# Kernel optimization log

Measured on AMD Instinct MI355X. Metric: run time of the kernel, lower is better.

Reference implementation:

```python
import jax, jax.numpy as jnp
import numpy as np

S, B, C, H, DH = 16, 16, 256, 4, 64
HW_TABLE, HW_HAND = 256, 36
HW = HW_TABLE + HW_HAND + 1  # 293 spatial tokens (table + hand + global)
LK = 128
MAX_T = 64
UH, UW, UC = 4, 4, 2
TH, TW, HH, HWW = 16, 16, 6, 6
N_MODES, N_SHAPES, N_COLORS = 20, 64, 16


def _ln(x, g, b):
    m = jnp.mean(x, -1, keepdims=True)
    v = jnp.var(x, -1, keepdims=True)
    return (x - m) / jnp.sqrt(v + 1e-5) * g + b


def _forward(tq, pad_q, xk, tk, pad_k,
             spatial_enc, temporal_enc, ln1_g, ln1_b,
             wq, bq, wk, bk, wv, bv, wo, bo, ln2_g, ln2_b,
             w1, b1, w2, b2, table_w, table_b, hand_w, hand_b,
             mode_w, mode_b, shape_w, shape_b, color_w, color_b):
    s, b = tq.shape
    Lq = s * HW
    # temporal + spatial positional broadcast-add -> padded query stream
    xt = temporal_enc[tq]                                        # (s,b,C)
    xq = (xt[:, None] + spatial_enc[None, :, None]).reshape(Lq, b, C)
    tq_e = jnp.broadcast_to(tq[:, None], (s, HW, b)).reshape(Lq, b)
    # padded causal mask: key visible iff tk <= tq, key in pad_k, query in pad_q*HW
    allowed = ((tk[None] <= tq_e[:, None])
               & (jnp.arange(LK)[None, :, None] < pad_k[None, None])
               & (jnp.arange(Lq)[:, None, None] < (pad_q * HW)[None, None]))  # (Lq,Lk,b)
    # cross-attention TransformerBlock (pre-LN MHA + FFN)
    qn = _ln(xq, ln1_g, ln1_b)
    Q = (qn @ wq + bq).reshape(Lq, b, H, DH)
    K = (xk @ wk + bk).reshape(LK, b, H, DH)
    V = (xk @ wv + bv).reshape(LK, b, H, DH)
    scores = jnp.einsum('qbhd,kbhd->bhqk', Q, K) / np.float32(np.sqrt(DH))
    scores = jnp.where(jnp.transpose(allowed, (2, 0, 1))[:, None], scores, jnp.float32(-1e9))
    a = jnp.einsum('bhqk,kbhd->qbhd', jax.nn.softmax(scores, -1), V).reshape(Lq, b, C)
    x = xq + a @ wo + bo
    x = x + jax.nn.gelu(_ln(x, ln2_g, ln2_b) @ w1 + b1) @ w2 + b2
    x = x.reshape(s, HW, b, C)
    # table decode: pixel-unshuffle (s,th,tw,b,uh,uw,uc) -> (s,b,uc,th*uh,tw*uw)
    tx = x[:, :HW_TABLE] @ table_w + table_b
    tx = tx.reshape(s, TH, TW, b, UH, UW, UC).transpose(0, 3, 6, 1, 4, 2, 5)
    tx = tx.reshape(s, b, UC, TH * UH, TW * UW)
    hx = x[:, HW_TABLE:HW_TABLE + HW_HAND] @ hand_w + hand_b
    hx = hx.reshape(s, HH, HWW, b, UH, UW, UC).transpose(0, 3, 6, 1, 4, 2, 5)
    hx = hx.reshape(s, b, UC, HH * UH, HWW * UW)
    gx = x[:, HW - 1]  # (s,b,C) global token
    return (gx @ mode_w + mode_b, gx @ shape_w + shape_b, gx @ color_w + color_b, tx, hx)


def setup_inputs():
    ks = jax.random.split(jax.random.key(0), 40)
    p = lambda k, shp: jax.random.normal(k, shp, jnp.float32) * 0.02
    inp = {}
    inp['tq'] = jnp.sort(jax.random.randint(ks[0], (S, B), 0, MAX_T), axis=0)
    inp['pad_q'] = jax.random.randint(ks[1], (B,), S // 2, S + 1)
    inp['xk'] = jax.random.normal(ks[2], (LK, B, C), jnp.float32)
    inp['tk'] = jnp.sort(jax.random.randint(ks[3], (LK, B), 0, MAX_T), axis=0).at[0].set(0)
    inp['pad_k'] = jax.random.randint(ks[4], (B,), LK // 2, LK + 1)
    inp['table_cursor_activate'] = jax.random.randint(ks[5], (S, B), 0, 2)
    inp['hand_cursor_activate'] = jax.random.randint(ks[6], (S, B), 0, 2)
    inp['insert_activate'] = jax.random.randint(ks[7], (S, B), 0, 2)
    inp['spatial_enc'] = p(ks[8], (HW, C))
    inp['temporal_enc'] = p(ks[9], (MAX_T, C))
    inp['ln1_g'] = jnp.ones(C); inp['ln1_b'] = jnp.zeros(C)
    inp['wq'] = p(ks[10], (C, C)); inp['bq'] = jnp.zeros(C)
    inp['wk'] = p(ks[11], (C, C)); inp['bk'] = jnp.zeros(C)
    inp['wv'] = p(ks[12], (C, C)); inp['bv'] = jnp.zeros(C)
    inp['wo'] = p(ks[13], (C, C)); inp['bo'] = jnp.zeros(C)
    inp['ln2_g'] = jnp.ones(C); inp['ln2_b'] = jnp.zeros(C)
    inp['w1'] = p(ks[14], (C, 4 * C)); inp['b1'] = jnp.zeros(4 * C)
    inp['w2'] = p(ks[15], (4 * C, C)); inp['b2'] = jnp.zeros(C)
    inp['table_w'] = p(ks[16], (C, UH * UW * UC)); inp['table_b'] = jnp.zeros(UH * UW * UC)
    inp['hand_w'] = p(ks[17], (C, UH * UW * UC)); inp['hand_b'] = jnp.zeros(UH * UW * UC)
    inp['mode_w'] = p(ks[18], (C, N_MODES)); inp['mode_b'] = jnp.zeros(N_MODES)
    inp['shape_w'] = p(ks[19], (C, N_SHAPES)); inp['shape_b'] = jnp.zeros(N_SHAPES)
    inp['color_w'] = p(ks[20], (C, N_COLORS)); inp['color_b'] = jnp.zeros(N_COLORS)
    return inp


def reference(tq, pad_q, xk, tk, pad_k, table_cursor_activate, hand_cursor_activate,
              insert_activate, spatial_enc, temporal_enc, ln1_g, ln1_b,
              wq, bq, wk, bk, wv, bv, wo, bo, ln2_g, ln2_b,
              w1, b1, w2, b2, table_w, table_b, hand_w, hand_b,
              mode_w, mode_b, shape_w, shape_b, color_w, color_b):
    # cursor/insert activates are unused in the old_style branch
    return _forward(tq, pad_q, xk, tk, pad_k, spatial_enc, temporal_enc,
                    ln1_g, ln1_b, wq, bq, wk, bk, wv, bv, wo, bo, ln2_g, ln2_b,
                    w1, b1, w2, b2, table_w, table_b, hand_w, hand_b,
                    mode_w, mode_b, shape_w, shape_b, color_w, color_b)
```

## Files before the change

### kernel.cpp

```cpp
#include <hip/hip_runtime.h>
#include <hip/hip_bf16.h>

namespace {
constexpr int cS = 16, cB = 16, cC = 256, cH = 4, cDH = 64, cHW = 293;
constexpr int cLQ = cS * cHW;
constexpr int cLK = 128;
constexpr int cNN = cLQ * cB;
constexpr size_t TX_OFF = 25600;
constexpr size_t HX_OFF = 2122752;
}

typedef unsigned short ushort_t;
typedef unsigned int uint_t;
typedef __attribute__((ext_vector_type(8))) short short8;
typedef __attribute__((ext_vector_type(4))) float f32x4;

__device__ __forceinline__ float bf2f(ushort_t u) {
  return __uint_as_float(((uint_t)u) << 16);
}
__device__ __forceinline__ ushort_t f2bf(float f) {
  __hip_bfloat16 h = __float2bfloat16(f);
  return *(ushort_t*)&h;
}

__device__ __forceinline__ size_t swz(int r, int c) {
  return (((size_t)(r >> 4) * 8 + (c >> 5)) * 64 + ((c >> 3) & 3) * 16 + (r & 15)) * 8 + (c & 7);
}

__global__ __launch_bounds__(256) void k_prep(
    const float* __restrict__ xk, ushort_t* __restrict__ xkb,
    const float* __restrict__ wq, ushort_t* __restrict__ wqs,
    const float* __restrict__ wk, ushort_t* __restrict__ wks,
    const float* __restrict__ wv, ushort_t* __restrict__ wvs,
    const float* __restrict__ wo, ushort_t* __restrict__ wos,
    const float* __restrict__ w1, ushort_t* __restrict__ w1s,
    const float* __restrict__ w2, ushort_t* __restrict__ w2s,
    const float* __restrict__ tw, ushort_t* __restrict__ tws,
    const float* __restrict__ hw_, ushort_t* __restrict__ hws)
{
  int bid = blockIdx.x;
  if (bid < 512) {
    int i4 = bid * 256 + threadIdx.x;
    int r = i4 >> 6;
    int c0 = (i4 & 63) * 4;
    float4 v = *(const float4*)(xk + (size_t)r * 256 + c0);
    ushort_t o[4] = {f2bf(v.x), f2bf(v.y), f2bf(v.z), f2bf(v.w)};
    *(uint2*)&xkb[swz(r, c0)] = *(uint2*)o;
    return;
  }
  int rr = bid - 512;
  const float* W; ushort_t* Ws; int N; int lb;
  if      (rr < 32)  { W = wq;  Ws = wqs; N = 256;  lb = rr; }
  else if (rr < 64)  { W = wk;  Ws = wks; N = 256;  lb = rr - 32; }
  else if (rr < 96)  { W = wv;  Ws = wvs; N = 256;  lb = rr - 64; }
  else if (rr < 128) { W = wo;  Ws = wos; N = 256;  lb = rr - 96; }
  else if (rr < 256) { W = w1;  Ws = w1s; N = 1024; lb = rr - 128; }
  else if (rr < 384) { W = w2;  Ws = w2s; N = 256;  lb = rr - 256; }
  else if (rr < 388) { W = tw;  Ws = tws; N = 32;   lb = rr - 384; }
  else               { W = hw_; Ws = hws; N = 32;   lb = rr - 388; }
  int slot = lb * 256 + threadIdx.x;
  int lane = slot & 63;
  int fr   = slot >> 6;
  int NB   = N >> 4;
  int nb   = fr % NB, kc = fr / NB;
  int n    = nb * 16 + (lane & 15);
  int k0   = kc * 32 + (lane >> 4) * 8;
  ushort_t tmp[8];
  #pragma unroll
  for (int i = 0; i < 8; ++i) tmp[i] = f2bf(W[(size_t)(k0 + i) * N + n]);
  *(uint4*)&Ws[(size_t)slot * 8] = *(uint4*)tmp;
}

__device__ __forceinline__ void gemm_k256(
    const ushort_t* __restrict__ A, const ushort_t* __restrict__ Ws,
    int rt0, int slot0, int NB, int lane, f32x4 c[4][4])
{
  #pragma unroll 2
  for (int kc = 0; kc < 8; ++kc) {
    short8 a[4];
    #pragma unroll
    for (int mf = 0; mf < 4; ++mf)
      a[mf] = *(const short8*)(A + (((size_t)(rt0 + mf) * 8 + kc) * 64 + lane) * 8);
    #pragma unroll
    for (int nb = 0; nb < 4; ++nb) {
      short8 b = *(const short8*)(Ws + (((size_t)kc * NB + slot0 + nb) * 64 + lane) * 8);
      #pragma unroll
      for (int mf = 0; mf < 4; ++mf)
        c[mf][nb] = __builtin_amdgcn_mfma_f32_16x16x32_bf16(a[mf], b, c[mf][nb], 0, 0, 0);
    }
  }
}

__global__ __launch_bounds__(256, 4) void k_qnp(
    const int* __restrict__ tq, const float* __restrict__ spatial,
    const float* __restrict__ temporal, const float* __restrict__ g,
    const float* __restrict__ bt, const ushort_t* __restrict__ Ws,
    const float* __restrict__ Bi, ushort_t* __restrict__ Out)
{
  __shared__ ushort_t aT[64 * 256];
  const int tid = threadIdx.x, lane = tid & 63, w = tid >> 6;
  const int rt0 = blockIdx.x * 4, row0 = blockIdx.x * 64;
  {
    int q = rt0 + w;
    int s = q / cHW, hw = q % cHW;
    int c0 = lane * 4;
    float4 sv = *(const float4*)(spatial + (size_t)hw * cC + c0);
    float4 g4 = *(const float4*)(g + c0);
    float4 b4 = *(const float4*)(bt + c0);
    int kc = c0 >> 5, qq = (c0 >> 3) & 3, joff = c0 & 7;
    for (int rr = 0; rr < 16; ++rr) {
      int t = tq[s * cB + rr];
      float4 tv = *(const float4*)(temporal + (size_t)t * cC + c0);
      float v0 = tv.x + sv.x, v1 = tv.y + sv.y, v2 = tv.z + sv.z, v3 = tv.w + sv.w;
      float sum = v0 + v1 + v2 + v3;
      float sum2 = v0 * v0 + v1 * v1 + v2 * v2 + v3 * v3;
      #pragma unroll
      for (int off = 32; off >= 1; off >>= 1) {
        sum  += __shfl_xor(sum,  off, 64);
        sum2 += __shfl_xor(sum2, off, 64);
      }
      float mean = sum * (1.0f / cC);
      float var  = sum2 * (1.0f / cC) - mean * mean;
      float inv  = rsqrtf(var + 1e-5f);
      ushort_t o[4] = {f2bf((v0 - mean) * inv * g4.x + b4.x),
                       f2bf((v1 - mean) * inv * g4.y + b4.y),
                       f2bf((v2 - mean) * inv * g4.z + b4.z),
                       f2bf((v3 - mean) * inv * g4.w + b4.w)};
      *(uint2*)&aT[(((w * 8 + kc) * 64) + qq * 16 + rr) * 8 + joff] = *(uint2*)o;
    }
  }
  __syncthreads();
  f32x4 z = {0.f, 0.f, 0.f, 0.f};
  f32x4 c[4][4];
  #pragma unroll
  for (int mf = 0; mf < 4; ++mf)
    #pragma unroll
    for (int nb = 0; nb < 4; ++nb) c[mf][nb] = z;
  gemm_k256(aT, Ws, 0, w * 4, 16, lane, c);
  const int lane15 = lane & 15, kq = lane >> 4;
  __syncthreads();
  #pragma unroll
  for (int nb = 0; nb < 4; ++nb) {
    int col = w * 64 + nb * 16 + lane15;
    float bias = Bi[col];
    #pragma unroll
    for (int mf = 0; mf < 4; ++mf)
      #pragma unroll
      for (int i = 0; i < 4; ++i)
        aT[(mf * 16 + kq * 4 + i) * 256 + col] = f2bf(c[mf][nb][i] + bias);
  }
  __syncthreads();
  uint2* outp = (uint2*)(Out + (size_t)row0 * 256);
  #pragma unroll
  for (int it = 0; it < 16; ++it) {
    int f = tid + it * 256;
    int row = f >> 6, c0 = (f & 63) * 4;
    outp[f] = *(uint2*)&aT[row * 256 + c0];
  }
}

__global__ __launch_bounds__(256, 4) void k_kv(
    const ushort_t* __restrict__ xkb, const ushort_t* __restrict__ wks,
    const ushort_t* __restrict__ wvs, const float* __restrict__ bk,
    const float* __restrict__ bv, ushort_t* __restrict__ Kb,
    ushort_t* __restrict__ Vb)
{
  const ushort_t* Ws = blockIdx.y ? wvs : wks;
  const float* Bi = blockIdx.y ? bv : bk;
  ushort_t* Out = blockIdx.y ? Vb : Kb;
  const int lane = threadIdx.x & 63, w = threadIdx.x >> 6;
  const int rt0 = blockIdx.x * 4, row0 = blockIdx.x * 64;
  f32x4 z = {0.f, 0.f, 0.f, 0.f};
  f32x4 c[4][4];
  #pragma unroll
  for (int mf = 0; mf < 4; ++mf)
    #pragma unroll
    for (int nb = 0; nb < 4; ++nb) c[mf][nb] = z;
  gemm_k256(xkb, Ws, rt0, w * 4, 16, lane, c);
  const int lane15 = lane & 15, kq = lane >> 4;
  #pragma unroll
  for (int nb = 0; nb < 4; ++nb) {
    int col = w * 64 + nb * 16 + lane15;
    float bias = Bi[col];
    #pragma unroll
    for (int mf = 0; mf < 4; ++mf)
      #pragma unroll
      for (int i = 0; i < 4; ++i) {
        int row = row0 + mf * 16 + kq * 4 + i;
        Out[(size_t)row * 256 + col] = f2bf(c[mf][nb][i] + bias);
      }
  }
}

__global__ __launch_bounds__(512, 4) void k_woffn(
    const ushort_t* __restrict__ A, const ushort_t* __restrict__ wos,
    const float* __restrict__ bo, const int* __restrict__ tq,
    const float* __restrict__ spatial, const float* __restrict__ temporal,
    const float* __restrict__ g, const float* __restrict__ bt,
    const ushort_t* __restrict__ w1s, const float* __restrict__ b1,
    const ushort_t* __restrict__ w2s, const float* __restrict__ b2,
    ushort_t* xres, ushort_t* __restrict__ x2out)
{
  __shared__ ushort_t aT[64 * 256];
  __shared__ ushort_t hL[64 * 256];
  __shared__ float red[8][64][2];
  __shared__ float meanL[64], invL[64];
  const int tid = threadIdx.x, lane = tid & 63, w = tid >> 6;
  const int lane15 = lane & 15, kq = lane >> 4;
  const int rt0 = blockIdx.x * 4, row0 = blockIdx.x * 64;
  const f32x4 z = {0.f, 0.f, 0.f, 0.f};

  f32x4 c[4][2];
  #pragma unroll
  for (int mf = 0; mf < 4; ++mf)
    #pragma unroll
    for (int nb = 0; nb < 2; ++nb) c[mf][nb] = z;
  #pragma unroll 1
  for (int kc = 0; kc < 8; ++kc) {
    short8 a[4];
    #pragma unroll
    for (int mf = 0; mf < 4; ++mf)
      a[mf] = *(const short8*)(A + (((size_t)(rt0 + mf) * 8 + kc) * 64 + lane) * 8);
    #pragma unroll
    for (int nb = 0; nb < 2; ++nb) {
      short8 b = *(const short8*)(wos + (((size_t)kc * 16 + w * 2 + nb) * 64 + lane) * 8);
      #pragma unroll
      for (int mf = 0; mf < 4; ++mf)
        c[mf][nb] = __builtin_amdgcn_mfma_f32_16x16x32_bf16(a[mf], b, c[mf][nb], 0, 0, 0);
    }
  }
  {
    int tt[4][4], hws[4];
    #pragma unroll
    for (int mf = 0; mf < 4; ++mf) {
      int q = rt0 + mf;
      int s = q / cHW;
      hws[mf] = q % cHW;
      #pragma unroll
      for (int i = 0; i < 4; ++i) tt[mf][i] = tq[s * cB + kq * 4 + i];
    }
    #pragma unroll
    for (int nb = 0; nb < 2; ++nb) {
      int col = w * 32 + nb * 16 + lane15;
      float bias = bo[col];
      #pragma unroll
      for (int mf = 0; mf < 4; ++mf) {
        float sp = spatial[(size_t)hws[mf] * cC + col];
        #pragma unroll
        for (int i = 0; i < 4; ++i)
          c[mf][nb][i] += bias + temporal[(size_t)tt[mf][i] * cC + col] + sp;
      }
    }
  }
  #pragma unroll
  for (int mf = 0; mf < 4; ++mf)
    #pragma unroll
    for (int i = 0; i < 4; ++i) {
      float s4 = c[mf][0][i] + c[mf][1][i];
      float q4 = c[mf][0][i] * c[mf][0][i] + c[mf][1][i] * c[mf][1][i];
      #pragma unroll
      for (int off = 8; off >= 1; off >>= 1) {
        s4 += __shfl_xor(s4, off, 64);
        q4 += __shfl_xor(q4, off, 64);
      }
      if (lane15 == 0) {
        red[w][mf * 16 + kq * 4 + i][0] = s4;
        red[w][mf * 16 + kq * 4 + i][1] = q4;
      }
    }
  __syncthreads();
  if (tid < 64) {
    float S = 0.f, Q = 0.f;
    #pragma unroll
    for (int ww = 0; ww < 8; ++ww) { S += red[ww][tid][0]; Q += red[ww][tid][1]; }
    float m = S * (1.0f / cC);
    float v = Q * (1.0f / cC) - m * m;
    meanL[tid] = m;
    invL[tid] = rsqrtf(v + 1e-5f);
  }
  __syncthreads();
  #pragma unroll
  for (int nb = 0; nb < 2; ++nb) {
    int col = w * 32 + nb * 16 + lane15;
    float gc = g[col], bc = bt[col];
    int qd = nb * 2 + (lane15 >> 3);
    int jd = lane15 & 7;
    #pragma unroll
    for (int mf = 0; mf < 4; ++mf)
      #pragma unroll
      for (int i = 0; i < 4; ++i) {
        int rl = mf * 16 + kq * 4 + i;
        float val = c[mf][nb][i];
        float lv = (val - meanL[rl]) * invL[rl] * gc + bc;
        aT[((mf * 8 + w) * 64 + qd * 16 + kq * 4 + i) * 8 + jd] = f2bf(lv);
        hL[rl * 256 + col] = f2bf(val);
      }
  }
  __syncthreads();
  {
    uint2* xw = (uint2*)(xres + (size_t)row0 * 256);
    #pragma unroll
    for (int it = 0; it < 8; ++it) {
      int f = tid + it * 512;
      int row = f >> 6, c0 = (f & 63) * 4;
      xw[f] = *(uint2*)&hL[row * 256 + c0];
    }
  }
  f32x4 c2[4][2];
  #pragma unroll
  for (int mf = 0; mf < 4; ++mf)
    #pragma unroll
    for (int nb = 0; nb < 2; ++nb) c2[mf][nb] = z;
  for (int hc = 0; hc < 4; ++hc) {
    f32x4 c1[4][2];
    #pragma unroll
    for (int mf = 0; mf < 4; ++mf)
      #pragma unroll
      for (int nb = 0; nb < 2; ++nb) c1[mf][nb] = z;
    #pragma unroll 1
    for (int kc = 0; kc < 8; ++kc) {
      short8 a[4];
      #pragma unroll
      for (int mf = 0; mf < 4; ++mf)
        a[mf] = *(const short8*)&aT[((mf * 8 + kc) * 64 + lane) * 8];
      #pragma unroll
      for (int nb = 0; nb < 2; ++nb) {
        int slot = hc * 16 + w * 2 + nb;
        short8 b = *(const short8*)(w1s + (((size_t)kc * 64 + slot) * 64 + lane) * 8);
        #pragma unroll
        for (int mf = 0; mf < 4; ++mf)
          c1[mf][nb] = __builtin_amdgcn_mfma_f32_16x16x32_bf16(a[mf], b, c1[mf][nb], 0, 0, 0);
      }
    }
    __syncthreads();
    #pragma unroll
    for (int nb = 0; nb < 2; ++nb) {
      int k2l = w * 32 + nb * 16 + lane15;
      float bias = b1[hc * 256 + k2l];
      int kc2l = k2l >> 5, kq2 = (k2l >> 3) & 3, j2 = k2l & 7;
      #pragma unroll
      for (int mf = 0; mf < 4; ++mf)
        #pragma unroll
        for (int i = 0; i < 4; ++i) {
          float xx = c1[mf][nb][i] + bias;
          float x2v = xx * xx;
          float mm = fmaf(x2v, 0.044715f, 1.0f);
          float u2 = xx * mm * -1.5957691216057308f;
          float e = __expf(u2);
          float ge = xx * __builtin_amdgcn_rcpf(1.0f + e);
          hL[(((kc2l * 4 + mf) * 64) + kq2 * 16 + kq * 4 + i) * 8 + j2] = f2bf(ge);
        }
    }
    __syncthreads();
    #pragma unroll 1
    for (int kc2 = 0; kc2 < 8; ++kc2) {
      short8 a2[4];
      #pragma unroll
      for (int mf = 0; mf < 4; ++mf)
        a2[mf] = *(const short8*)&hL[((kc2 * 4 + mf) * 64 + lane) * 8];
      #pragma unroll
      for (int nb = 0; nb < 2; ++nb) {
        short8 b = *(const short8*)(w2s +
            (((size_t)(hc * 8 + kc2) * 16 + w * 2 + nb) * 64 + lane) * 8);
        #pragma unroll
        for (int mf = 0; mf < 4; ++mf)
          c2[mf][nb] = __builtin_amdgcn_mfma_f32_16x16x32_bf16(a2[mf], b, c2[mf][nb], 0, 0, 0);
      }
    }
  }
  __syncthreads();
  #pragma unroll
  for (int nb = 0; nb < 2; ++nb) {
    int col = w * 32 + nb * 16 + lane15;
    float bias = b2[col];
    #pragma unroll
    for (int mf = 0; mf < 4; ++mf)
      #pragma unroll
      for (int i = 0; i < 4; ++i)
        aT[(mf * 16 + kq * 4 + i) * 256 + col] = f2bf(c2[mf][nb][i] + bias);
  }
  __syncthreads();
  {
    const int rt = (tid + 256) & 511;
    uint2* xp = (uint2*)(x2out + (size_t)row0 * 256);
    const uint2* xr = (const uint2*)(xres + (size_t)row0 * 256);
    #pragma unroll
    for (int it = 0; it < 8; ++it) {
      int f = rt + it * 512;
      int row = f >> 6, c0 = (f & 63) * 4;
      uint2 hv = *(uint2*)&aT[row * 256 + c0];
      uint2 rv = xr[f];
      const ushort_t* hp = (const ushort_t*)&hv;
      const ushort_t* rp = (const ushort_t*)&rv;
      ushort_t o[4];
      #pragma unroll
      for (int j = 0; j < 4; ++j) o[j] = f2bf(bf2f(hp[j]) + bf2f(rp[j]));
      xp[f] = *(uint2*)o;
    }
  }
}

__global__ __launch_bounds__(512, 4) void k_attn(
    const ushort_t* __restrict__ Qb, const ushort_t* __restrict__ Kb,
    const ushort_t* __restrict__ Vb, const int* __restrict__ tq,
    const int* __restrict__ tk, const int* __restrict__ pad_q,
    const int* __restrict__ pad_k, ushort_t* __restrict__ aout)
{
  __shared__ ushort_t KL[128 * 72];
  __shared__ ushort_t VtL[64 * 136];
  __shared__ ushort_t pL[8][16 * 136];
  __shared__ int tkL[128];

  const int h = blockIdx.y, b = blockIdx.z;
  const int tid = threadIdx.x, lane = tid & 63, w = tid >> 6;
  const int m15 = lane & 15, quad = lane >> 4;

  for (int i = tid; i < 128 * 16; i += 512) {
    int k = i >> 4, d4 = (i & 15) * 4;
    size_t src = (size_t)(k * cB + b) * 256 + h * 64 + d4;
    uint2 kv = *(const uint2*)&Kb[src];
    uint2 vv = *(const uint2*)&Vb[src];
    *(uint2*)&KL[k * 72 + d4] = kv;
    const ushort_t* vvp = (const ushort_t*)&vv;
    #pragma unroll
    for (int t = 0; t < 4; ++t) VtL[(d4 + t) * 136 + k] = vvp[t];
  }
  if (tid < 128) tkL[tid] = tk[tid * cB + b];
  __syncthreads();
  const int pk = pad_k[b];
  const int pq = pad_q[b] * cHW;
  ushort_t* pRow = pL[w];
  const f32x4 z = {0.f, 0.f, 0.f, 0.f};

  for (int pr = 0; pr < 4; ++pr) {
    int qt = blockIdx.x * 32 + pr * 8 + w;
    if (qt >= 293) break;
    const ushort_t* qrow =
        Qb + ((size_t)((qt * 16 + m15) * cB + b)) * 256 + h * 64 + quad * 8;
    short8 qa0 = *(const short8*)(qrow);
    short8 qa1 = *(const short8*)(qrow + 32);
    f32x4 s[8];
    #pragma unroll
    for (int nf = 0; nf < 8; ++nf) {
      const ushort_t* kp = KL + (nf * 16 + m15) * 72 + quad * 8;
      short8 b0 = *(const short8*)(kp);
      short8 b1 = *(const short8*)(kp + 32);
      s[nf] = __builtin_amdgcn_mfma_f32_16x16x32_bf16(qa0, b0, z, 0, 0, 0);
      s[nf] = __builtin_amdgcn_mfma_f32_16x16x32_bf16(qa1, b1, s[nf], 0, 0, 0);
    }
    int tqv[4], qok[4];
    #pragma unroll
    for (int i = 0; i < 4; ++i) {
      int qg = qt * 16 + quad * 4 + i;
      int sidx = (qg * 3579) >> 20;
      tqv[i] = tq[sidx * cB + b];
      qok[i] = (qg < pq);
    }
    #pragma unroll
    for (int nf = 0; nf < 8; ++nf) {
      int kidx = nf * 16 + m15;
      int tkc = tkL[kidx];
      bool kok = (kidx < pk);
      #pragma unroll
      for (int i = 0; i < 4; ++i) {
        bool ok = kok && qok[i] && (tkc <= tqv[i]);
        s[nf][i] = ok ? s[nf][i] * 0.125f : -1e9f;
      }
    }
    float mx[4], l[4];
    #pragma unroll
    for (int i = 0; i < 4; ++i) {
      float m = s[0][i];
      #pragma unroll
      for (int nf = 1; nf < 8; ++nf) m = fmaxf(m, s[nf][i]);
      #pragma unroll
      for (int off = 8; off >= 1; off >>= 1) m = fmaxf(m, __shfl_xor(m, off, 64));
      mx[i] = m;
    }
    #pragma unroll
    for (int i = 0; i < 4; ++i) l[i] = 0.f;
    #pragma unroll
    for (int nf = 0; nf < 8; ++nf)
      #pragma unroll
      for (int i = 0; i < 4; ++i) {
        float p = __expf(s[nf][i] - mx[i]);
        s[nf][i] = p;
        l[i] += p;
      }
    #pragma unroll
    for (int i = 0; i < 4; ++i) {
      float t = l[i];
      #pragma unroll
      for (int off = 8; off >= 1; off >>= 1) t += __shfl_xor(t, off, 64);
      l[i] = 1.0f / t;
    }
    #pragma unroll
    for (int nf = 0; nf < 8; ++nf)
      #pragma unroll
      for (int i = 0; i < 4; ++i)
        pRow[(quad * 4 + i) * 136 + nf * 16 + m15] = f2bf(s[nf][i]);
    f32x4 o[4];
    #pragma unroll
    for (int nf = 0; nf < 4; ++nf) o[nf] = z;
    #pragma unroll
    for (int kc = 0; kc < 4; ++kc) {
      short8 pa = *(const short8*)(pRow + m15 * 136 + kc * 32 + quad * 8);
      #pragma unroll
      for (int nf = 0; nf < 4; ++nf) {
        short8 vb = *(const short8*)(VtL + (nf * 16 + m15) * 136 + kc * 32 + quad * 8);
        o[nf] = __builtin_amdgcn_mfma_f32_16x16x32_bf16(pa, vb, o[nf], 0, 0, 0);
      }
    }
    #pragma unroll
    for (int nf = 0; nf < 4; ++nf) {
      int c = h * 64 + nf * 16 + m15;
      size_t base = ((size_t)(c >> 5)) * 64 + ((c >> 3) & 3) * 16 + b;
      int cj = c & 7;
      #pragma unroll
      for (int i = 0; i < 4; ++i) {
        int qg = qt * 16 + quad * 4 + i;
        aout[(((size_t)qg * 8) * 64 + base) * 8 + cj] = f2bf(o[nf][i] * l[i]);
      }
    }
  }
}

__global__ __launch_bounds__(256, 4) void k_thm(
    const ushort_t* __restrict__ x2, const ushort_t* __restrict__ tws,
    const float* __restrict__ tb, const ushort_t* __restrict__ hws,
    const float* __restrict__ hb, float* __restrict__ out)
{
  __shared__ ushort_t aT[64 * 264];
  const int tid = threadIdx.x, lane = tid & 63, w = tid >> 6;
  const int m15 = lane & 15, quad = lane >> 4;
  const int row0 = blockIdx.x * 64;
  #pragma unroll
  for (int it = 0; it < 8; ++it) {
    int f = tid + it * 256;
    int row = f >> 5, cb = f & 31;
    *(uint4*)&aT[row * 264 + cb * 8] =
        *(const uint4*)&x2[(size_t)(row0 + row) * 256 + cb * 8];
  }
  __syncthreads();
  const f32x4 z = {0.f, 0.f, 0.f, 0.f};
  f32x4 ct[2], ch[2];
  ct[0] = ct[1] = ch[0] = ch[1] = z;
  const ushort_t* arow = aT + (w * 16 + m15) * 264 + quad * 8;
  #pragma unroll
  for (int kc = 0; kc < 8; ++kc) {
    short8 a = *(const short8*)(arow + kc * 32);
    #pragma unroll
    for (int nb = 0; nb < 2; ++nb) {
      short8 bt_ = *(const short8*)(tws + (((size_t)(kc * 2 + nb)) * 64 + lane) * 8);
      short8 bh_ = *(const short8*)(hws + (((size_t)(kc * 2 + nb)) * 64 + lane) * 8);
      ct[nb] = __builtin_amdgcn_mfma_f32_16x16x32_bf16(a, bt_, ct[nb], 0, 0, 0);
      ch[nb] = __builtin_amdgcn_mfma_f32_16x16x32_bf16(a, bh_, ch[nb], 0, 0, 0);
    }
  }
  #pragma unroll
  for (int nb = 0; nb < 2; ++nb) {
    int j = nb * 16 + m15;
    float tbias = tb[j], hbias = hb[j];
    int uh = j >> 3, uw = (j >> 1) & 3, uc = j & 1;
    #pragma unroll
    for (int i = 0; i < 4; ++i) {
      int rg = row0 + w * 16 + quad * 4 + i;
      int b = rg & 15, q = rg >> 4;
      int s = (q * 3579) >> 20;
      int hw = q - s * cHW;
      if (hw < 256) {
        int th = hw >> 4, twi = hw & 15;
        size_t idx = TX_OFF +
            ((((size_t)(s * cB + b)) * 2 + uc) * 64 + (th * 4 + uh)) * 64 + (twi * 4 + uw);
        out[idx] = ct[nb][i] + tbias;
      } else if (hw < 292) {
        int h2 = hw - 256;
        int hh = h2 / 6, ww = h2 % 6;
        size_t idx = HX_OFF +
            ((((size_t)(s * cB + b)) * 2 + uc) * 24 + (hh * 4 + uh)) * 24 + (ww * 4 + uw);
        out[idx] = ch[nb][i] + hbias;
      }
    }
  }
}

__global__ __launch_bounds__(128) void k_gx(
    const ushort_t* __restrict__ x2,
    const float* __restrict__ mw, const float* __restrict__ mbi,
    const float* __restrict__ sw, const float* __restrict__ sbi,
    const float* __restrict__ cw, const float* __restrict__ cbi,
    float* __restrict__ out)
{
  int sb = blockIdx.x;
  int s = sb >> 4, b = sb & 15;
  __shared__ float rowL[256];
  const ushort_t* row = x2 + ((size_t)(s * cHW + 292) * cB + b) * cC;
  for (int i = threadIdx.x; i < 256; i += 128) rowL[i] = bf2f(row[i]);
  __syncthreads();
  int j = threadIdx.x;
  if (j < 100) {
    const float* W;
    const float* Bi;
    int jj, M;
    size_t off;
    if (j < 20)      { W = mw; Bi = mbi; jj = j;      M = 20; off = 0;     }
    else if (j < 84) { W = sw; Bi = sbi; jj = j - 20; M = 64; off = 5120;  }
    else             { W = cw; Bi = cbi; jj = j - 84; M = 16; off = 21504; }
    float acc = Bi[jj];
    for (int c = 0; c < 256; ++c) acc = fmaf(rowL[c], W[c * M + jj], acc);
    out[off + (size_t)sb * M + jj] = acc;
  }
}

extern "C" void kernel_launch(void* const* d_in, const int* in_sizes, int n_in,
                              void* d_out, int out_size, void* d_ws, size_t ws_size,
                              hipStream_t stream)
{
  const int*   tq       = (const int*)d_in[0];
  const int*   pad_q    = (const int*)d_in[1];
  const float* xk       = (const float*)d_in[2];
  const int*   tk       = (const int*)d_in[3];
  const int*   pad_k    = (const int*)d_in[4];
  const float* spatial  = (const float*)d_in[8];
  const float* temporal = (const float*)d_in[9];
  const float* ln1_g    = (const float*)d_in[10];
  const float* ln1_b    = (const float*)d_in[11];
  const float* wq       = (const float*)d_in[12];
  const float* bq       = (const float*)d_in[13];
  const float* wk       = (const float*)d_in[14];
  const float* bk       = (const float*)d_in[15];
  const float* wv       = (const float*)d_in[16];
  const float* bv       = (const float*)d_in[17];
  const float* wo       = (const float*)d_in[18];
  const float* bo       = (const float*)d_in[19];
  const float* ln2_g    = (const float*)d_in[20];
  const float* ln2_b    = (const float*)d_in[21];
  const float* w1       = (const float*)d_in[22];
  const float* b1       = (const float*)d_in[23];
  const float* w2       = (const float*)d_in[24];
  const float* b2       = (const float*)d_in[25];
  const float* table_w  = (const float*)d_in[26];
  const float* table_b  = (const float*)d_in[27];
  const float* hand_w   = (const float*)d_in[28];
  const float* hand_b   = (const float*)d_in[29];
  const float* mode_w   = (const float*)d_in[30];
  const float* mode_b   = (const float*)d_in[31];
  const float* shape_w  = (const float*)d_in[32];
  const float* shape_b  = (const float*)d_in[33];
  const float* color_w  = (const float*)d_in[34];
  const float* color_b  = (const float*)d_in[35];
  float* out = (float*)d_out;

  char* ws = (char*)d_ws;
  const size_t NB2 = (size_t)cNN * cC * sizeof(ushort_t);
  ushort_t* buf1 = (ushort_t*)ws;
  ushort_t* buf2 = (ushort_t*)(ws + NB2);
  char* p = ws + 2 * NB2;
  ushort_t* Kb  = (ushort_t*)p;  p += (size_t)cLK * cB * 256 * 2;
  ushort_t* Vb  = (ushort_t*)p;  p += (size_t)cLK * cB * 256 * 2;
  ushort_t* xkb = (ushort_t*)p;  p += (size_t)cLK * cB * 256 * 2;
  ushort_t* wqs = (ushort_t*)p;  p += 256 * 256 * 2;
  ushort_t* wks = (ushort_t*)p;  p += 256 * 256 * 2;
  ushort_t* wvs = (ushort_t*)p;  p += 256 * 256 * 2;
  ushort_t* wos = (ushort_t*)p;  p += 256 * 256 * 2;
  ushort_t* w1s = (ushort_t*)p;  p += 256 * 1024 * 2;
  ushort_t* w2s = (ushort_t*)p;  p += 1024 * 256 * 2;
  ushort_t* tws = (ushort_t*)p;  p += 256 * 32 * 2;
  ushort_t* hws = (ushort_t*)p;  p += 256 * 32 * 2;

  k_prep<<<904, 256, 0, stream>>>(xk, xkb, wq, wqs, wk, wks, wv, wvs,
                                  wo, wos, w1, w1s, w2, w2s,
                                  table_w, tws, hand_w, hws);
  k_kv<<<dim3(32, 2), 256, 0, stream>>>(xkb, wks, wvs, bk, bv, Kb, Vb);
  k_qnp<<<cNN / 64, 256, 0, stream>>>(tq, spatial, temporal, ln1_g, ln1_b,
                                      wqs, bq, buf2);
  k_attn<<<dim3(10, cH, cB), 512, 0, stream>>>(buf2, Kb, Vb, tq, tk,
                                               pad_q, pad_k, buf1);
  k_woffn<<<cNN / 64, 512, 0, stream>>>(buf1, wos, bo, tq, spatial, temporal,
                                        ln2_g, ln2_b, w1s, b1, w2s, b2,
                                        buf1, buf2);
  k_thm<<<cNN / 64, 256, 0, stream>>>(buf2, tws, table_b, hws, hand_b, out);
  k_gx<<<cS * cB, 128, 0, stream>>>(buf2, mode_w, mode_b, shape_w, shape_b,
                                    color_w, color_b, out);
}
```

Before: 435.1 us.

## Split FFN first GEMM into halves and merge global heads into table/hand kernel

In the fused Wo+FFN kernel, each 256-wide hidden chunk is now computed in two 16-column halves, with the GELU write for each half issued right after it. This halves the live c1 accumulator registers, which may help occupancy, and lets the first half's GELU overlap the second half's MFMAs. Separately, the small mode/shape/color head kernel is folded into the table/hand decode kernel as extra blocks, removing one launch. The extra blocks use the 256-thread shape, so some threads sit idle in the tail work.

```diff
diff --git a/kernel.cpp b/kernel.cpp
--- a/kernel.cpp
+++ b/kernel.cpp
@@ -312,44 +312,41 @@
     #pragma unroll
     for (int nb = 0; nb < 2; ++nb) c2[mf][nb] = z;
   for (int hc = 0; hc < 4; ++hc) {
-    f32x4 c1[4][2];
-    #pragma unroll
-    for (int mf = 0; mf < 4; ++mf)
-      #pragma unroll
-      for (int nb = 0; nb < 2; ++nb) c1[mf][nb] = z;
-    #pragma unroll 1
-    for (int kc = 0; kc < 8; ++kc) {
-      short8 a[4];
-      #pragma unroll
-      for (int mf = 0; mf < 4; ++mf)
-        a[mf] = *(const short8*)&aT[((mf * 8 + kc) * 64 + lane) * 8];
-      #pragma unroll
-      for (int nb = 0; nb < 2; ++nb) {
-        int slot = hc * 16 + w * 2 + nb;
+    #pragma unroll
+    for (int half = 0; half < 2; ++half) {
+      f32x4 c1[4];
+      #pragma unroll
+      for (int mf = 0; mf < 4; ++mf) c1[mf] = z;
+      #pragma unroll 1
+      for (int kc = 0; kc < 8; ++kc) {
+        short8 a[4];
+        #pragma unroll
+        for (int mf = 0; mf < 4; ++mf)
+          a[mf] = *(const short8*)&aT[((mf * 8 + kc) * 64 + lane) * 8];
+        int slot = hc * 16 + w * 2 + half;
         short8 b = *(const short8*)(w1s + (((size_t)kc * 64 + slot) * 64 + lane) * 8);
         #pragma unroll
         for (int mf = 0; mf < 4; ++mf)
-          c1[mf][nb] = __builtin_amdgcn_mfma_f32_16x16x32_bf16(a[mf], b, c1[mf][nb], 0, 0, 0);
-      }
-    }
-    __syncthreads();
-    #pragma unroll
-    for (int nb = 0; nb < 2; ++nb) {
-      int k2l = w * 32 + nb * 16 + lane15;
-      float bias = b1[hc * 256 + k2l];
-      int kc2l = k2l >> 5, kq2 = (k2l >> 3) & 3, j2 = k2l & 7;
-      #pragma unroll
-      for (int mf = 0; mf < 4; ++mf)
+          c1[mf] = __builtin_amdgcn_mfma_f32_16x16x32_bf16(a[mf], b, c1[mf], 0, 0, 0);
+      }
+      if (half == 0) __syncthreads();
+      {
+        int k2l = w * 32 + half * 16 + lane15;
+        float bias = b1[hc * 256 + k2l];
+        int kc2l = k2l >> 5, kq2 = (k2l >> 3) & 3, j2 = k2l & 7;
         #pragma unroll
-        for (int i = 0; i < 4; ++i) {
-          float xx = c1[mf][nb][i] + bias;
-          float x2v = xx * xx;
-          float mm = fmaf(x2v, 0.044715f, 1.0f);
-          float u2 = xx * mm * -1.5957691216057308f;
-          float e = __expf(u2);
-          float ge = xx * __builtin_amdgcn_rcpf(1.0f + e);
-          hL[(((kc2l * 4 + mf) * 64) + kq2 * 16 + kq * 4 + i) * 8 + j2] = f2bf(ge);
-        }
+        for (int mf = 0; mf < 4; ++mf)
+          #pragma unroll
+          for (int i = 0; i < 4; ++i) {
+            float xx = c1[mf][i] + bias;
+            float x2v = xx * xx;
+            float mm = fmaf(x2v, 0.044715f, 1.0f);
+            float u2 = xx * mm * -1.5957691216057308f;
+            float e = __expf(u2);
+            float ge = xx * __builtin_amdgcn_rcpf(1.0f + e);
+            hL[(((kc2l * 4 + mf) * 64) + kq2 * 16 + kq * 4 + i) * 8 + j2] = f2bf(ge);
+          }
+      }
     }
     __syncthreads();
     #pragma unroll 1
@@ -525,13 +522,41 @@
   }
 }
 
-__global__ __launch_bounds__(256, 4) void k_thm(
+__global__ __launch_bounds__(256, 4) void k_thg(
     const ushort_t* __restrict__ x2, const ushort_t* __restrict__ tws,
     const float* __restrict__ tb, const ushort_t* __restrict__ hws,
-    const float* __restrict__ hb, float* __restrict__ out)
+    const float* __restrict__ hb,
+    const float* __restrict__ mw, const float* __restrict__ mbi,
+    const float* __restrict__ sw, const float* __restrict__ sbi,
+    const float* __restrict__ cw, const float* __restrict__ cbi,
+    float* __restrict__ out)
 {
   __shared__ ushort_t aT[64 * 264];
-  const int tid = threadIdx.x, lane = tid & 63, w = tid >> 6;
+  const int NTH = cNN / 64;
+  const int tid = threadIdx.x;
+  if ((int)blockIdx.x >= NTH) {
+    int sb = blockIdx.x - NTH;
+    int s = sb >> 4, b = sb & 15;
+    float* rowL = (float*)aT;
+    const ushort_t* row = x2 + ((size_t)(s * cHW + 292) * cB + b) * cC;
+    if (tid < 256) rowL[tid] = bf2f(row[tid]);
+    __syncthreads();
+    int j = tid;
+    if (j < 100) {
+      const float* W;
+      const float* Bi;
+      int jj, M;
+      size_t off;
+      if (j < 20)      { W = mw; Bi = mbi; jj = j;      M = 20; off = 0;     }
+      else if (j < 84) { W = sw; Bi = sbi; jj = j - 20; M = 64; off = 5120;  }
+      else             { W = cw; Bi = cbi; jj = j - 84; M = 16; off = 21504; }
+      float acc = Bi[jj];
+      for (int c = 0; c < 256; ++c) acc = fmaf(rowL[c], W[c * M + jj], acc);
+      out[off + (size_t)sb * M + jj] = acc;
+    }
+    return;
+  }
+  const int lane = tid & 63, w = tid >> 6;
   const int m15 = lane & 15, quad = lane >> 4;
   const int row0 = blockIdx.x * 64;
   #pragma unroll
@@ -581,34 +606,6 @@
         out[idx] = ch[nb][i] + hbias;
       }
     }
-  }
-}
-
-__global__ __launch_bounds__(128) void k_gx(
-    const ushort_t* __restrict__ x2,
-    const float* __restrict__ mw, const float* __restrict__ mbi,
-    const float* __restrict__ sw, const float* __restrict__ sbi,
-    const float* __restrict__ cw, const float* __restrict__ cbi,
-    float* __restrict__ out)
-{
-  int sb = blockIdx.x;
-  int s = sb >> 4, b = sb & 15;
-  __shared__ float rowL[256];
-  const ushort_t* row = x2 + ((size_t)(s * cHW + 292) * cB + b) * cC;
-  for (int i = threadIdx.x; i < 256; i += 128) rowL[i] = bf2f(row[i]);
-  __syncthreads();
-  int j = threadIdx.x;
-  if (j < 100) {
-    const float* W;
-    const float* Bi;
-    int jj, M;
-    size_t off;
-    if (j < 20)      { W = mw; Bi = mbi; jj = j;      M = 20; off = 0;     }
-    else if (j < 84) { W = sw; Bi = sbi; jj = j - 20; M = 64; off = 5120;  }
-    else             { W = cw; Bi = cbi; jj = j - 84; M = 16; off = 21504; }
-    float acc = Bi[jj];
-    for (int c = 0; c < 256; ++c) acc = fmaf(rowL[c], W[c * M + jj], acc);
-    out[off + (size_t)sb * M + jj] = acc;
   }
 }
 
@@ -679,7 +676,7 @@
   k_woffn<<<cNN / 64, 512, 0, stream>>>(buf1, wos, bo, tq, spatial, temporal,
                                         ln2_g, ln2_b, w1s, b1, w2s, b2,
                                         buf1, buf2);
-  k_thm<<<cNN / 64, 256, 0, stream>>>(buf2, tws, table_b, hws, hand_b, out);
-  k_gx<<<cS * cB, 128, 0, stream>>>(buf2, mode_w, mode_b, shape_w, shape_b,
-                                    color_w, color_b, out);
-}
+  k_thg<<<cNN / 64 + cS * cB, 256, 0, stream>>>(buf2, tws, table_b, hws, hand_b,
+                                                mode_w, mode_b, shape_w, shape_b,
+                                                color_w, color_b, out);
+}
```

Result: faster. 417.9 us (-3.9%).
